# Optimization experiments

Measured on AMD Instinct MI355X. Metric: run time of the kernel, lower is better.

## Reference

```python
import jax, jax.numpy as jnp
import numpy as np

B, K = 16384, 32          # batch, negatives_per_sample
LATENT, ACT, H, Q = 256, 64, 128, 65536
EPS = 0.01                # label smoothing


def _san(x):
    # sanitize_tensor: replace non-finite with 0.0
    return jnp.nan_to_num(x, nan=0.0, posinf=0.0, neginf=0.0)


def _mlp(x, w1, b1, w2, b2):
    return jnp.maximum(x @ w1 + b1, 0.0) @ w2 + b2


def setup_inputs() -> dict:
    key = jax.random.key(0)
    ks = jax.random.split(key, 12)
    s = 0.02
    return {
        "action": jax.random.normal(ks[0], (B, ACT), jnp.float32),
        "latent": jax.random.normal(ks[1], (B, LATENT), jnp.float32),
        "queue": jax.random.normal(ks[2], (Q, LATENT), jnp.float32),
        "neg_idx": jax.random.randint(ks[3], (B, K), 0, Q, jnp.int32),
        "a_w1": jax.random.normal(ks[4], (ACT, H), jnp.float32) * s,
        "a_b1": jnp.zeros((H,), jnp.float32),
        "a_w2": jax.random.normal(ks[5], (H, H), jnp.float32) * s,
        "a_b2": jnp.zeros((H,), jnp.float32),
        "l_w1": jax.random.normal(ks[6], (LATENT, H), jnp.float32) * s,
        "l_b1": jnp.zeros((H,), jnp.float32),
        "l_w2": jax.random.normal(ks[7], (H, H), jnp.float32) * s,
        "l_b2": jnp.zeros((H,), jnp.float32),
        "temperature": jnp.float32(0.1),
    }


def reference(action, latent, queue, neg_idx, a_w1, a_b1, a_w2, a_b2,
              l_w1, l_b1, l_w2, l_b2, temperature):
    action = _san(action).astype(jnp.float32)
    latent = _san(latent).astype(jnp.float32)

    emb_a = _san(_mlp(action, a_w1, a_b1, a_w2, a_b2))      # [B,H]
    emb_l = _san(_mlp(latent, l_w1, l_b1, l_w2, l_b2))      # [B,H]

    # replay-queue gather of negatives, projected (detached in original)
    sampled = jax.lax.stop_gradient(queue[neg_idx])          # [B,K,LATENT]
    neg = _san(_mlp(sampled.reshape(-1, LATENT), l_w1, l_b1, l_w2, l_b2)
               .reshape(B, K, H))                            # [B,K,H]

    all_lat = jnp.concatenate([emb_l[:, None, :], neg], axis=1)  # [B,K+1,H]

    temp = jnp.clip(jnp.nan_to_num(temperature, nan=0.1, posinf=0.1, neginf=0.1),
                    0.01, 10.0)
    logits = jnp.einsum('bd,bnd->bn', emb_a, all_lat) / temp
    logits = jnp.clip(_san(logits), -20.0, 20.0)             # [B,K+1]

    # cross-entropy vs label 0 with label smoothing 0.01, reduction='none'
    logp = jax.nn.log_softmax(logits, axis=-1)
    loss = -(1.0 - EPS) * logp[:, 0] - EPS * logp.mean(axis=-1)
    loss = _san(loss)
    return -jnp.clip(loss, -10.0, 10.0)                      # [B]
```

## Files before the change

kernel.cpp:

```cpp
#include <hip/hip_runtime.h>
#include <hip/hip_bf16.h>

#define NB   16384
#define KNEG 32
#define LQ   256
#define LACT 64
#define HD   128
#define QN   65536
#define EPS_ 0.01f

typedef __attribute__((ext_vector_type(8))) short s16x8;
typedef __attribute__((ext_vector_type(4))) float f32x4;

__device__ __forceinline__ float san(float x) { return isfinite(x) ? x : 0.0f; }

__device__ __forceinline__ ushort bfbits(float f) {
    uint u = __builtin_bit_cast(uint, f);
    u += 0x7FFFu + ((u >> 16) & 1u);
    return (ushort)(u >> 16);
}
__device__ __forceinline__ float bf2f(ushort h) {
    uint u = ((uint)h) << 16;
    return __builtin_bit_cast(float, u);
}

__global__ __launch_bounds__(256) void prep_weights(
    const float* __restrict__ aw1, const float* __restrict__ aw2,
    const float* __restrict__ lw1, const float* __restrict__ lw2,
    ushort* __restrict__ aw1T, ushort* __restrict__ aw2T,
    ushort* __restrict__ lw1T, ushort* __restrict__ lw2T)
{
    int idx = blockIdx.x * 256 + threadIdx.x;
    if (idx < 8192) {
        int r = idx >> 7, c = idx & 127;
        aw1T[c * 64 + r] = bfbits(aw1[idx]);
    } else if (idx < 24576) {
        int e = idx - 8192, r = e >> 7, c = e & 127;
        aw2T[c * 128 + r] = bfbits(aw2[e]);
    } else if (idx < 57344) {
        int e = idx - 24576, r = e >> 7, c = e & 127;
        lw1T[c * 256 + r] = bfbits(lw1[e]);
    } else {
        int e = idx - 57344, r = e >> 7, c = e & 127;
        lw2T[c * 128 + r] = bfbits(lw2[e]);
    }
}

template<int L>
__device__ __forceinline__ void mlp_tile(
    const float* __restrict__ Xt,  const ushort* __restrict__ W1T,
    const float* __restrict__ b1,  const ushort* __restrict__ W2T,
    const float* __restrict__ b2,  ushort* __restrict__ outT,
    char* hb, int w, int g, int c)
{
    const int swz = 16 * (c & 7);

    f32x4 acc[2][8];
    #pragma unroll
    for (int r = 0; r < 2; ++r)
        #pragma unroll
        for (int mt = 0; mt < 8; ++mt) acc[r][mt] = (f32x4)(0.0f);

    #pragma unroll
    for (int ks = 0; ks < L / 32; ++ks) {
        s16x8 bx[2];
        #pragma unroll
        for (int r = 0; r < 2; ++r) {
            const float* xr = Xt + (size_t)(w * 32 + r * 16 + c) * L + 32 * ks + 8 * g;
            float4 xa = *(const float4*)xr;
            float4 xb = *(const float4*)(xr + 4);
            bx[r][0] = (short)bfbits(san(xa.x)); bx[r][1] = (short)bfbits(san(xa.y));
            bx[r][2] = (short)bfbits(san(xa.z)); bx[r][3] = (short)bfbits(san(xa.w));
            bx[r][4] = (short)bfbits(san(xb.x)); bx[r][5] = (short)bfbits(san(xb.y));
            bx[r][6] = (short)bfbits(san(xb.z)); bx[r][7] = (short)bfbits(san(xb.w));
        }
        #pragma unroll
        for (int mt = 0; mt < 8; ++mt) {
            s16x8 af = *(const s16x8*)(W1T + (16 * mt + c) * L + 32 * ks + 8 * g);
            acc[0][mt] = __builtin_amdgcn_mfma_f32_16x16x32_bf16(af, bx[0], acc[0][mt], 0, 0, 0);
            acc[1][mt] = __builtin_amdgcn_mfma_f32_16x16x32_bf16(af, bx[1], acc[1][mt], 0, 0, 0);
        }
    }

    #pragma unroll
    for (int r = 0; r < 2; ++r)
        #pragma unroll
        for (int mt = 0; mt < 8; ++mt) {
            float4 bb = *(const float4*)(b1 + 16 * mt + 4 * g);
            ushort4 hv;
            hv.x = bfbits(fmaxf(acc[r][mt][0] + bb.x, 0.0f));
            hv.y = bfbits(fmaxf(acc[r][mt][1] + bb.y, 0.0f));
            hv.z = bfbits(fmaxf(acc[r][mt][2] + bb.z, 0.0f));
            hv.w = bfbits(fmaxf(acc[r][mt][3] + bb.w, 0.0f));
            int off = (32 * mt + 8 * g) ^ swz;
            *(ushort4*)(hb + (r * 16 + c) * 256 + off) = hv;
        }
    __syncthreads();

    f32x4 acc2[2][8];
    #pragma unroll
    for (int r = 0; r < 2; ++r)
        #pragma unroll
        for (int mt = 0; mt < 8; ++mt) acc2[r][mt] = (f32x4)(0.0f);

    #pragma unroll
    for (int ks = 0; ks < 4; ++ks) {
        s16x8 hf[2];
        #pragma unroll
        for (int r = 0; r < 2; ++r) {
            int off = (64 * ks + 16 * g) ^ swz;
            hf[r] = *(const s16x8*)(hb + (r * 16 + c) * 256 + off);
        }
        #pragma unroll
        for (int mt = 0; mt < 8; ++mt) {
            s16x8 af = *(const s16x8*)(W2T + (16 * mt + c) * HD + 32 * ks + 8 * g);
            acc2[0][mt] = __builtin_amdgcn_mfma_f32_16x16x32_bf16(af, hf[0], acc2[0][mt], 0, 0, 0);
            acc2[1][mt] = __builtin_amdgcn_mfma_f32_16x16x32_bf16(af, hf[1], acc2[1][mt], 0, 0, 0);
        }
    }

    #pragma unroll
    for (int r = 0; r < 2; ++r) {
        ushort* orow = outT + (size_t)(w * 32 + r * 16 + c) * HD;
        #pragma unroll
        for (int mt = 0; mt < 8; ++mt) {
            float4 bb = *(const float4*)(b2 + 16 * mt + 4 * g);
            ushort4 ov;
            ov.x = bfbits(san(acc2[r][mt][0] + bb.x));
            ov.y = bfbits(san(acc2[r][mt][1] + bb.y));
            ov.z = bfbits(san(acc2[r][mt][2] + bb.z));
            ov.w = bfbits(san(acc2[r][mt][3] + bb.w));
            *(ushort4*)(orow + 16 * mt + 4 * g) = ov;
        }
    }
}

__global__ __launch_bounds__(256) void mlp_fused(
    const float* __restrict__ queue, const float* __restrict__ latent,
    const float* __restrict__ action,
    const ushort* __restrict__ lw1T, const float* __restrict__ lb1,
    const ushort* __restrict__ lw2T, const float* __restrict__ lb2,
    const ushort* __restrict__ aw1T, const float* __restrict__ ab1,
    const ushort* __restrict__ aw2T, const float* __restrict__ ab2,
    ushort* __restrict__ proj_q, ushort* __restrict__ emb_l,
    ushort* __restrict__ emb_a)
{
    __shared__ char hsm[4][8192];
    const int tid  = threadIdx.x;
    const int w    = tid >> 6;
    const int lane = tid & 63;
    const int g    = lane >> 4;
    const int c    = lane & 15;
    char* hb = &hsm[w][0];

    const int tile = blockIdx.x;
    if (tile < 512) {
        mlp_tile<LQ>(queue + (size_t)tile * 128 * LQ, lw1T, lb1, lw2T, lb2,
                     proj_q + (size_t)tile * 128 * HD, hb, w, g, c);
    } else if (tile < 640) {
        int t = tile - 512;
        mlp_tile<LQ>(latent + (size_t)t * 128 * LQ, lw1T, lb1, lw2T, lb2,
                     emb_l + (size_t)t * 128 * HD, hb, w, g, c);
    } else {
        int t = tile - 640;
        mlp_tile<LACT>(action + (size_t)t * 128 * LACT, aw1T, ab1, aw2T, ab2,
                       emb_a + (size_t)t * 128 * HD, hb, w, g, c);
    }
}

__global__ __launch_bounds__(256) void loss_kernel(
    const ushort* __restrict__ emb_a, const ushort* __restrict__ emb_l,
    const ushort* __restrict__ proj_q, const int* __restrict__ neg_idx,
    const float* __restrict__ temp_p, float* __restrict__ out)
{
    __shared__ float eas[4][2][128];

    const int tid  = threadIdx.x;
    const int w    = tid >> 6;
    const int lane = tid & 63;
    const int h    = lane >> 5;
    const int j    = lane & 31;
    const long b   = (long)blockIdx.x * 8 + w * 2 + h;

    float t = temp_p[0];
    if (!isfinite(t)) t = 0.1f;
    t = fminf(fmaxf(t, 0.01f), 10.0f);
    const float invt = 1.0f / t;

    ushort4 av = ((const ushort4*)(emb_a + b * HD))[j];
    ushort4 lv = ((const ushort4*)(emb_l + b * HD))[j];
    float a0 = bf2f(av.x), a1 = bf2f(av.y), a2 = bf2f(av.z), a3 = bf2f(av.w);
    *(float4*)&eas[w][h][4 * j] = make_float4(a0, a1, a2, a3);
    float posp = a0 * bf2f(lv.x) + a1 * bf2f(lv.y) + a2 * bf2f(lv.z) + a3 * bf2f(lv.w);
    const int nidx = neg_idx[b * KNEG + j];
    __syncthreads();

    const ushort* nrow = proj_q + (long)nidx * HD;
    float acc = 0.0f;
    #pragma unroll
    for (int i = 0; i < 16; ++i) {
        s16x8 v = *(const s16x8*)(nrow + i * 8);
        #pragma unroll
        for (int k = 0; k < 8; ++k)
            acc = fmaf(bf2f((ushort)v[k]), eas[w][h][i * 8 + k], acc);
    }

    #pragma unroll
    for (int off = 1; off < 32; off <<= 1) posp += __shfl_xor(posp, off, 64);

    float lgp = fminf(fmaxf(san(posp * invt), -20.0f), 20.0f);
    float lgn = fminf(fmaxf(san(acc  * invt), -20.0f), 20.0f);

    float m = fmaxf(lgp, lgn);
    #pragma unroll
    for (int off = 1; off < 32; off <<= 1) m = fmaxf(m, __shfl_xor(m, off, 64));

    float e  = expf(lgn - m);
    float sl = lgn;
    #pragma unroll
    for (int off = 1; off < 32; off <<= 1) {
        e  += __shfl_xor(e, off, 64);
        sl += __shfl_xor(sl, off, 64);
    }
    e  += expf(lgp - m);
    sl += lgp;

    float loss = (m + logf(e)) - (1.0f - EPS_) * lgp - EPS_ * (sl * (1.0f / 33.0f));
    loss = fminf(fmaxf(san(loss), -10.0f), 10.0f);

    if (j == 0) out[b] = -loss;
}

extern "C" void kernel_launch(void* const* d_in, const int* in_sizes, int n_in,
                              void* d_out, int out_size, void* d_ws, size_t ws_size,
                              hipStream_t stream) {
    const float* action  = (const float*)d_in[0];
    const float* latent  = (const float*)d_in[1];
    const float* queue   = (const float*)d_in[2];
    const int*   neg_idx = (const int*)  d_in[3];
    const float* a_w1    = (const float*)d_in[4];
    const float* a_b1    = (const float*)d_in[5];
    const float* a_w2    = (const float*)d_in[6];
    const float* a_b2    = (const float*)d_in[7];
    const float* l_w1    = (const float*)d_in[8];
    const float* l_b1    = (const float*)d_in[9];
    const float* l_w2    = (const float*)d_in[10];
    const float* l_b2    = (const float*)d_in[11];
    const float* temp    = (const float*)d_in[12];
    float* out = (float*)d_out;

    ushort* emb_a  = (ushort*)d_ws;
    ushort* emb_l  = emb_a + (size_t)NB * HD;
    ushort* proj_q = emb_l + (size_t)NB * HD;
    ushort* aw1T   = proj_q + (size_t)QN * HD;
    ushort* aw2T   = aw1T + 128 * 64;
    ushort* lw1T   = aw2T + 128 * 128;
    ushort* lw2T   = lw1T + 128 * 256;

    prep_weights<<<288, 256, 0, stream>>>(a_w1, a_w2, l_w1, l_w2, aw1T, aw2T, lw1T, lw2T);
    mlp_fused<<<768, 256, 0, stream>>>(queue, latent, action,
                                       lw1T, l_b1, lw2T, l_b2,
                                       aw1T, a_b1, aw2T, a_b2,
                                       proj_q, emb_l, emb_a);
    loss_kernel<<<NB / 8, 256, 0, stream>>>(emb_a, emb_l, proj_q, neg_idx, temp, out);
}
```

Measured before the change: 207.8 us.

## Rewrite MLP as persistent kernel with register-resident weights and prefetch

Replaces the per-tile fused MLP with a persistent grid-stride kernel. Each wave keeps its slice of the bf16 W1/W2 fragments in registers, inputs are staged through swizzled LDS in 16-row tiles, and the next tile's input is prefetched into registers while the current one computes. The action MLP moves into its own launch. The weight transpose is vectorized to four rows per thread, and the loss dot product uses four independent accumulators with vector LDS reads. This trades one extra launch and smaller per-block tiles (more barriers per row) for removing repeated weight loads from global memory and for overlapping input loads with compute.

```diff
diff --git a/kernel.cpp b/kernel.cpp
--- a/kernel.cpp
+++ b/kernel.cpp
@@ -12,6 +12,8 @@
 typedef __attribute__((ext_vector_type(8))) short s16x8;
 typedef __attribute__((ext_vector_type(4))) float f32x4;
 
+#define MFMA __builtin_amdgcn_mfma_f32_16x16x32_bf16
+
 __device__ __forceinline__ float san(float x) { return isfinite(x) ? x : 0.0f; }
 
 __device__ __forceinline__ ushort bfbits(float f) {
@@ -22,6 +24,12 @@
 __device__ __forceinline__ float bf2f(ushort h) {
     uint u = ((uint)h) << 16;
     return __builtin_bit_cast(float, u);
+}
+__device__ __forceinline__ ushort4 cvt4(float4 v) {
+    ushort4 r;
+    r.x = bfbits(san(v.x)); r.y = bfbits(san(v.y));
+    r.z = bfbits(san(v.z)); r.w = bfbits(san(v.w));
+    return r;
 }
 
 __global__ __launch_bounds__(256) void prep_weights(
@@ -30,145 +38,162 @@
     ushort* __restrict__ aw1T, ushort* __restrict__ aw2T,
     ushort* __restrict__ lw1T, ushort* __restrict__ lw2T)
 {
-    int idx = blockIdx.x * 256 + threadIdx.x;
-    if (idx < 8192) {
-        int r = idx >> 7, c = idx & 127;
-        aw1T[c * 64 + r] = bfbits(aw1[idx]);
-    } else if (idx < 24576) {
-        int e = idx - 8192, r = e >> 7, c = e & 127;
-        aw2T[c * 128 + r] = bfbits(aw2[e]);
-    } else if (idx < 57344) {
-        int e = idx - 24576, r = e >> 7, c = e & 127;
-        lw1T[c * 256 + r] = bfbits(lw1[e]);
-    } else {
-        int e = idx - 57344, r = e >> 7, c = e & 127;
-        lw2T[c * 128 + r] = bfbits(lw2[e]);
-    }
+    int t = blockIdx.x * 256 + threadIdx.x;
+    const float* src; ushort* dst; int R;
+    if      (t <  2048) {             src = aw1; dst = aw1T; R = 64;  }
+    else if (t <  6144) { t -= 2048;  src = aw2; dst = aw2T; R = 128; }
+    else if (t < 14336) { t -= 6144;  src = lw1; dst = lw1T; R = 256; }
+    else if (t < 18432) { t -= 14336; src = lw2; dst = lw2T; R = 128; }
+    else return;
+    int c = t & 127, r4 = t >> 7;
+    ushort4 o;
+    o.x = bfbits(src[(4 * r4 + 0) * 128 + c]);
+    o.y = bfbits(src[(4 * r4 + 1) * 128 + c]);
+    o.z = bfbits(src[(4 * r4 + 2) * 128 + c]);
+    o.w = bfbits(src[(4 * r4 + 3) * 128 + c]);
+    *(ushort4*)(dst + c * R + 4 * r4) = o;
 }
 
 template<int L>
-__device__ __forceinline__ void mlp_tile(
-    const float* __restrict__ Xt,  const ushort* __restrict__ W1T,
-    const float* __restrict__ b1,  const ushort* __restrict__ W2T,
-    const float* __restrict__ b2,  ushort* __restrict__ outT,
-    char* hb, int w, int g, int c)
+__global__ __launch_bounds__(256, 3) void mlp_v4(
+    const float* __restrict__ X0, const float* __restrict__ X1, int rows0,
+    ushort* __restrict__ out0, ushort* __restrict__ out1,
+    const ushort* __restrict__ W1T, const float* __restrict__ b1,
+    const ushort* __restrict__ W2T, const float* __restrict__ b2,
+    int ntiles)
 {
-    const int swz = 16 * (c & 7);
-
-    f32x4 acc[2][8];
-    #pragma unroll
-    for (int r = 0; r < 2; ++r)
-        #pragma unroll
-        for (int mt = 0; mt < 8; ++mt) acc[r][mt] = (f32x4)(0.0f);
-
-    #pragma unroll
-    for (int ks = 0; ks < L / 32; ++ks) {
-        s16x8 bx[2];
-        #pragma unroll
-        for (int r = 0; r < 2; ++r) {
-            const float* xr = Xt + (size_t)(w * 32 + r * 16 + c) * L + 32 * ks + 8 * g;
-            float4 xa = *(const float4*)xr;
-            float4 xb = *(const float4*)(xr + 4);
-            bx[r][0] = (short)bfbits(san(xa.x)); bx[r][1] = (short)bfbits(san(xa.y));
-            bx[r][2] = (short)bfbits(san(xa.z)); bx[r][3] = (short)bfbits(san(xa.w));
-            bx[r][4] = (short)bfbits(san(xb.x)); bx[r][5] = (short)bfbits(san(xb.y));
-            bx[r][6] = (short)bfbits(san(xb.z)); bx[r][7] = (short)bfbits(san(xb.w));
-        }
-        #pragma unroll
-        for (int mt = 0; mt < 8; ++mt) {
-            s16x8 af = *(const s16x8*)(W1T + (16 * mt + c) * L + 32 * ks + 8 * g);
-            acc[0][mt] = __builtin_amdgcn_mfma_f32_16x16x32_bf16(af, bx[0], acc[0][mt], 0, 0, 0);
-            acc[1][mt] = __builtin_amdgcn_mfma_f32_16x16x32_bf16(af, bx[1], acc[1][mt], 0, 0, 0);
-        }
-    }
-
-    #pragma unroll
-    for (int r = 0; r < 2; ++r)
-        #pragma unroll
-        for (int mt = 0; mt < 8; ++mt) {
-            float4 bb = *(const float4*)(b1 + 16 * mt + 4 * g);
-            ushort4 hv;
-            hv.x = bfbits(fmaxf(acc[r][mt][0] + bb.x, 0.0f));
-            hv.y = bfbits(fmaxf(acc[r][mt][1] + bb.y, 0.0f));
-            hv.z = bfbits(fmaxf(acc[r][mt][2] + bb.z, 0.0f));
-            hv.w = bfbits(fmaxf(acc[r][mt][3] + bb.w, 0.0f));
-            int off = (32 * mt + 8 * g) ^ swz;
-            *(ushort4*)(hb + (r * 16 + c) * 256 + off) = hv;
-        }
-    __syncthreads();
-
-    f32x4 acc2[2][8];
-    #pragma unroll
-    for (int r = 0; r < 2; ++r)
-        #pragma unroll
-        for (int mt = 0; mt < 8; ++mt) acc2[r][mt] = (f32x4)(0.0f);
-
-    #pragma unroll
-    for (int ks = 0; ks < 4; ++ks) {
-        s16x8 hf[2];
-        #pragma unroll
-        for (int r = 0; r < 2; ++r) {
-            int off = (64 * ks + 16 * g) ^ swz;
-            hf[r] = *(const s16x8*)(hb + (r * 16 + c) * 256 + off);
-        }
-        #pragma unroll
-        for (int mt = 0; mt < 8; ++mt) {
-            s16x8 af = *(const s16x8*)(W2T + (16 * mt + c) * HD + 32 * ks + 8 * g);
-            acc2[0][mt] = __builtin_amdgcn_mfma_f32_16x16x32_bf16(af, hf[0], acc2[0][mt], 0, 0, 0);
-            acc2[1][mt] = __builtin_amdgcn_mfma_f32_16x16x32_bf16(af, hf[1], acc2[1][mt], 0, 0, 0);
-        }
-    }
-
-    #pragma unroll
-    for (int r = 0; r < 2; ++r) {
-        ushort* orow = outT + (size_t)(w * 32 + r * 16 + c) * HD;
-        #pragma unroll
-        for (int mt = 0; mt < 8; ++mt) {
-            float4 bb = *(const float4*)(b2 + 16 * mt + 4 * g);
-            ushort4 ov;
-            ov.x = bfbits(san(acc2[r][mt][0] + bb.x));
-            ov.y = bfbits(san(acc2[r][mt][1] + bb.y));
-            ov.z = bfbits(san(acc2[r][mt][2] + bb.z));
-            ov.w = bfbits(san(acc2[r][mt][3] + bb.w));
-            *(ushort4*)(orow + 16 * mt + 4 * g) = ov;
-        }
-    }
-}
-
-__global__ __launch_bounds__(256) void mlp_fused(
-    const float* __restrict__ queue, const float* __restrict__ latent,
-    const float* __restrict__ action,
-    const ushort* __restrict__ lw1T, const float* __restrict__ lb1,
-    const ushort* __restrict__ lw2T, const float* __restrict__ lb2,
-    const ushort* __restrict__ aw1T, const float* __restrict__ ab1,
-    const ushort* __restrict__ aw2T, const float* __restrict__ ab2,
-    ushort* __restrict__ proj_q, ushort* __restrict__ emb_l,
-    ushort* __restrict__ emb_a)
-{
-    __shared__ char hsm[4][8192];
+    constexpr int KS1  = L / 32;
+    constexpr int SWZM = (L == 64) ? 7 : 15;
+    constexpr int PFN  = (L == 64) ? 1 : 4;
+
+    __shared__ __align__(16) char xb[16 * 2 * L];
+    __shared__ __align__(16) char hb[16 * 256];
+
     const int tid  = threadIdx.x;
     const int w    = tid >> 6;
     const int lane = tid & 63;
     const int g    = lane >> 4;
     const int c    = lane & 15;
-    char* hb = &hsm[w][0];
-
-    const int tile = blockIdx.x;
-    if (tile < 512) {
-        mlp_tile<LQ>(queue + (size_t)tile * 128 * LQ, lw1T, lb1, lw2T, lb2,
-                     proj_q + (size_t)tile * 128 * HD, hb, w, g, c);
-    } else if (tile < 640) {
-        int t = tile - 512;
-        mlp_tile<LQ>(latent + (size_t)t * 128 * LQ, lw1T, lb1, lw2T, lb2,
-                     emb_l + (size_t)t * 128 * HD, hb, w, g, c);
-    } else {
-        int t = tile - 640;
-        mlp_tile<LACT>(action + (size_t)t * 128 * LACT, aw1T, ab1, aw2T, ab2,
-                       emb_a + (size_t)t * 128 * HD, hb, w, g, c);
-    }
-}
-
-__global__ __launch_bounds__(256) void loss_kernel(
+    const int mtg0 = 2 * w, mtg1 = 2 * w + 1;
+
+    s16x8 w1f[KS1][2], w2f[4][2];
+    #pragma unroll
+    for (int ks = 0; ks < KS1; ++ks) {
+        w1f[ks][0] = *(const s16x8*)(W1T + (16 * mtg0 + c) * L + 32 * ks + 8 * g);
+        w1f[ks][1] = *(const s16x8*)(W1T + (16 * mtg1 + c) * L + 32 * ks + 8 * g);
+    }
+    #pragma unroll
+    for (int ks = 0; ks < 4; ++ks) {
+        w2f[ks][0] = *(const s16x8*)(W2T + (16 * mtg0 + c) * HD + 32 * ks + 8 * g);
+        w2f[ks][1] = *(const s16x8*)(W2T + (16 * mtg1 + c) * HD + 32 * ks + 8 * g);
+    }
+
+    const int srow = tid >> 4;
+    const int scol = tid & 15;
+
+    float4 pf[PFN];
+
+    auto src_ptr = [&](int tt) -> const float* {
+        int r0 = tt * 16;
+        const float* base = (r0 < rows0) ? X0 + (size_t)r0 * L
+                                         : X1 + (size_t)(r0 - rows0) * L;
+        return base + srow * L + scol * (L / 16);
+    };
+
+    int tt = blockIdx.x;
+    if (tt < ntiles) {
+        const float* p = src_ptr(tt);
+        #pragma unroll
+        for (int q = 0; q < PFN; ++q) pf[q] = ((const float4*)p)[q];
+    }
+
+    for (; tt < ntiles; tt += gridDim.x) {
+        if constexpr (L == 256) {
+            ushort4 q0 = cvt4(pf[0]), q1 = cvt4(pf[1]);
+            ushort4 q2 = cvt4(pf[2]), q3 = cvt4(pf[3]);
+            s16x8 v0 = { (short)q0.x, (short)q0.y, (short)q0.z, (short)q0.w,
+                         (short)q1.x, (short)q1.y, (short)q1.z, (short)q1.w };
+            s16x8 v1 = { (short)q2.x, (short)q2.y, (short)q2.z, (short)q2.w,
+                         (short)q3.x, (short)q3.y, (short)q3.z, (short)q3.w };
+            int a  = srow * 512 + scol * 32;
+            int sz = srow << 4;
+            *(s16x8*)(xb + ( a        ^ sz)) = v0;
+            *(s16x8*)(xb + ((a + 16)  ^ sz)) = v1;
+        } else {
+            ushort4 q0 = cvt4(pf[0]);
+            int a  = srow * 128 + scol * 8;
+            int sz = (srow & 7) << 4;
+            *(ushort4*)(xb + (a ^ sz)) = q0;
+        }
+        asm volatile("s_waitcnt lgkmcnt(0)" ::: "memory");
+        __builtin_amdgcn_s_barrier();
+
+        int nt = tt + gridDim.x;
+        if (nt < ntiles) {
+            const float* p = src_ptr(nt);
+            #pragma unroll
+            for (int q = 0; q < PFN; ++q) pf[q] = ((const float4*)p)[q];
+        }
+
+        f32x4 acc0 = (f32x4)(0.0f), acc1 = (f32x4)(0.0f);
+        #pragma unroll
+        for (int ks = 0; ks < KS1; ++ks) {
+            int a = (c * 2 * L + 64 * ks + 16 * g) ^ ((c & SWZM) << 4);
+            s16x8 bx = *(const s16x8*)(xb + a);
+            acc0 = MFMA(w1f[ks][0], bx, acc0, 0, 0, 0);
+            acc1 = MFMA(w1f[ks][1], bx, acc1, 0, 0, 0);
+        }
+
+        {
+            float4 bb0 = *(const float4*)(b1 + 16 * mtg0 + 4 * g);
+            float4 bb1v = *(const float4*)(b1 + 16 * mtg1 + 4 * g);
+            ushort4 h0, h1;
+            h0.x = bfbits(fmaxf(acc0[0] + bb0.x, 0.0f));
+            h0.y = bfbits(fmaxf(acc0[1] + bb0.y, 0.0f));
+            h0.z = bfbits(fmaxf(acc0[2] + bb0.z, 0.0f));
+            h0.w = bfbits(fmaxf(acc0[3] + bb0.w, 0.0f));
+            h1.x = bfbits(fmaxf(acc1[0] + bb1v.x, 0.0f));
+            h1.y = bfbits(fmaxf(acc1[1] + bb1v.y, 0.0f));
+            h1.z = bfbits(fmaxf(acc1[2] + bb1v.z, 0.0f));
+            h1.w = bfbits(fmaxf(acc1[3] + bb1v.w, 0.0f));
+            *(ushort4*)(hb + ((c * 256 + (16 * mtg0 + 4 * g) * 2) ^ (c << 4))) = h0;
+            *(ushort4*)(hb + ((c * 256 + (16 * mtg1 + 4 * g) * 2) ^ (c << 4))) = h1;
+        }
+        asm volatile("s_waitcnt lgkmcnt(0)" ::: "memory");
+        __builtin_amdgcn_s_barrier();
+
+        f32x4 d0 = (f32x4)(0.0f), d1 = (f32x4)(0.0f);
+        #pragma unroll
+        for (int ks = 0; ks < 4; ++ks) {
+            int a = (c * 256 + 64 * ks + 16 * g) ^ (c << 4);
+            s16x8 hx = *(const s16x8*)(hb + a);
+            d0 = MFMA(w2f[ks][0], hx, d0, 0, 0, 0);
+            d1 = MFMA(w2f[ks][1], hx, d1, 0, 0, 0);
+        }
+
+        {
+            int r0 = tt * 16;
+            ushort* orow = ((r0 < rows0) ? out0 + (size_t)r0 * HD
+                                         : out1 + (size_t)(r0 - rows0) * HD)
+                           + (size_t)c * HD;
+            float4 c0 = *(const float4*)(b2 + 16 * mtg0 + 4 * g);
+            float4 c1 = *(const float4*)(b2 + 16 * mtg1 + 4 * g);
+            ushort4 o0, o1;
+            o0.x = bfbits(san(d0[0] + c0.x));
+            o0.y = bfbits(san(d0[1] + c0.y));
+            o0.z = bfbits(san(d0[2] + c0.z));
+            o0.w = bfbits(san(d0[3] + c0.w));
+            o1.x = bfbits(san(d1[0] + c1.x));
+            o1.y = bfbits(san(d1[1] + c1.y));
+            o1.z = bfbits(san(d1[2] + c1.z));
+            o1.w = bfbits(san(d1[3] + c1.w));
+            *(ushort4*)(orow + 16 * mtg0 + 4 * g) = o0;
+            *(ushort4*)(orow + 16 * mtg1 + 4 * g) = o1;
+        }
+    }
+}
+
+__global__ __launch_bounds__(256, 6) void loss_v2(
     const ushort* __restrict__ emb_a, const ushort* __restrict__ emb_l,
     const ushort* __restrict__ proj_q, const int* __restrict__ neg_idx,
     const float* __restrict__ temp_p, float* __restrict__ out)
@@ -192,18 +217,31 @@
     float a0 = bf2f(av.x), a1 = bf2f(av.y), a2 = bf2f(av.z), a3 = bf2f(av.w);
     *(float4*)&eas[w][h][4 * j] = make_float4(a0, a1, a2, a3);
     float posp = a0 * bf2f(lv.x) + a1 * bf2f(lv.y) + a2 * bf2f(lv.z) + a3 * bf2f(lv.w);
-    const int nidx = neg_idx[b * KNEG + j];
+    const int ni = neg_idx[b * KNEG + j];
     __syncthreads();
 
-    const ushort* nrow = proj_q + (long)nidx * HD;
-    float acc = 0.0f;
-    #pragma unroll
-    for (int i = 0; i < 16; ++i) {
-        s16x8 v = *(const s16x8*)(nrow + i * 8);
-        #pragma unroll
-        for (int k = 0; k < 8; ++k)
-            acc = fmaf(bf2f((ushort)v[k]), eas[w][h][i * 8 + k], acc);
-    }
+    const ushort* nrow = proj_q + (long)ni * HD;
+    float ac0 = 0.0f, ac1 = 0.0f, ac2 = 0.0f, ac3 = 0.0f;
+    #pragma unroll
+    for (int bt = 0; bt < 2; ++bt) {
+        s16x8 v[8];
+        #pragma unroll
+        for (int q = 0; q < 8; ++q) v[q] = ((const s16x8*)nrow)[bt * 8 + q];
+        #pragma unroll
+        for (int q = 0; q < 8; ++q) {
+            float4 ea = *(const float4*)&eas[w][h][(bt * 8 + q) * 8];
+            float4 eb = *(const float4*)&eas[w][h][(bt * 8 + q) * 8 + 4];
+            ac0 = fmaf(bf2f((ushort)v[q][0]), ea.x, ac0);
+            ac1 = fmaf(bf2f((ushort)v[q][1]), ea.y, ac1);
+            ac2 = fmaf(bf2f((ushort)v[q][2]), ea.z, ac2);
+            ac3 = fmaf(bf2f((ushort)v[q][3]), ea.w, ac3);
+            ac0 = fmaf(bf2f((ushort)v[q][4]), eb.x, ac0);
+            ac1 = fmaf(bf2f((ushort)v[q][5]), eb.y, ac1);
+            ac2 = fmaf(bf2f((ushort)v[q][6]), eb.z, ac2);
+            ac3 = fmaf(bf2f((ushort)v[q][7]), eb.w, ac3);
+        }
+    }
+    float acc = (ac0 + ac1) + (ac2 + ac3);
 
     #pragma unroll
     for (int off = 1; off < 32; off <<= 1) posp += __shfl_xor(posp, off, 64);
@@ -257,10 +295,13 @@
     ushort* lw1T   = aw2T + 128 * 128;
     ushort* lw2T   = lw1T + 128 * 256;
 
-    prep_weights<<<288, 256, 0, stream>>>(a_w1, a_w2, l_w1, l_w2, aw1T, aw2T, lw1T, lw2T);
-    mlp_fused<<<768, 256, 0, stream>>>(queue, latent, action,
-                                       lw1T, l_b1, lw2T, l_b2,
-                                       aw1T, a_b1, aw2T, a_b2,
-                                       proj_q, emb_l, emb_a);
-    loss_kernel<<<NB / 8, 256, 0, stream>>>(emb_a, emb_l, proj_q, neg_idx, temp, out);
-}
+    prep_weights<<<72, 256, 0, stream>>>(a_w1, a_w2, l_w1, l_w2,
+                                         aw1T, aw2T, lw1T, lw2T);
+    mlp_v4<LQ><<<768, 256, 0, stream>>>(queue, latent, QN, proj_q, emb_l,
+                                        lw1T, l_b1, lw2T, l_b2,
+                                        (QN + NB) / 16);
+    mlp_v4<LACT><<<768, 256, 0, stream>>>(action, action, NB, emb_a, emb_a,
+                                          aw1T, a_b1, aw2T, a_b2,
+                                          NB / 16);
+    loss_v2<<<NB / 8, 256, 0, stream>>>(emb_a, emb_l, proj_q, neg_idx, temp, out);
+}
```

Result: faster. 182.7 us (-12.1%).
